# Performance work log

Measured on AMD Instinct MI355X. Metric: run time of the kernel, lower is better.

Reference implementation:

```python
import jax, jax.numpy as jnp
import numpy as np


def _gcn_conv(x, edge_index, W, b):
    # PyG GCNConv: linear transform, add self-loops, symmetric deg^{-1/2} norm,
    # scatter-add aggregation from source (row) into target (col), then bias.
    N = x.shape[0]
    h = x @ W  # [N, out]
    loops = jnp.arange(N, dtype=edge_index.dtype)
    row = jnp.concatenate([edge_index[0], loops])  # sources j
    col = jnp.concatenate([edge_index[1], loops])  # targets i
    deg = jax.ops.segment_sum(jnp.ones_like(col, dtype=h.dtype), col, num_segments=N)
    dinv = jnp.where(deg > 0, jax.lax.rsqrt(deg), 0.0)
    norm = dinv[row] * dinv[col]  # [E+N]
    msgs = norm[:, None] * h[row]  # gather + scale
    out = jax.ops.segment_sum(msgs, col, num_segments=N)  # scatter-add
    return out + b


def setup_inputs() -> dict:
    key = jax.random.key(0)
    k1, k2, k3, k4 = jax.random.split(key, 4)
    N, E, F, H = 100000, 3200000, 128, 64
    x = jax.random.normal(k1, (N, F), dtype=jnp.float32)
    edge_index = jax.random.randint(k2, (2, E), 0, N, dtype=jnp.int64)
    W1 = jax.random.normal(k3, (F, H), dtype=jnp.float32) * (1.0 / np.sqrt(F))
    b1 = jnp.zeros((H,), dtype=jnp.float32)
    W2 = jax.random.normal(k4, (H, 1), dtype=jnp.float32) * (1.0 / np.sqrt(H))
    b2 = jnp.zeros((1,), dtype=jnp.float32)
    return {"x": x, "edge_index": edge_index, "W1": W1, "b1": b1, "W2": W2, "b2": b2}


def reference(x, edge_index, W1, b1, W2, b2):
    # eval mode: dropout is identity
    h = _gcn_conv(x, edge_index, W1, b1)
    h = jax.nn.relu(h)
    h = _gcn_conv(h, edge_index, W2, b2)  # [N, 1]
    return jnp.mean(h, axis=0)  # [1]
```

## Files before the change

kernel.cpp:

```cpp
#include <hip/hip_runtime.h>
#include <hip/hip_bf16.h>
#include <stdint.h>


#define F_IN 128
#define H_DIM 64
#define BKT_SH 8
#define BKT_SZ 256
#define MAXBKT 512
#define PWG 256
#define PTHR 256
#define PPTHR 512
#define TILE 4096
#define CSR_CAP 10240
#define FINBLK 2048

typedef int   i4 __attribute__((ext_vector_type(4)));
typedef float f4 __attribute__((ext_vector_type(4)));
typedef float fv2 __attribute__((ext_vector_type(2)));

#if defined(__has_builtin)
#if __has_builtin(__builtin_amdgcn_cvt_pk_f32_fp8) && __has_builtin(__builtin_amdgcn_cvt_pk_fp8_f32)
#define HW_FP8 1
#endif
#endif

__device__ __forceinline__ float sw_dec_e4m3(unsigned b) {
    unsigned s = b & 0x80, e = (b >> 3) & 15, mm = b & 7;
    float v;
    if (e) v = __uint_as_float(((e + 120u) << 23) | (mm << 20));
    else   v = (float)mm * 0.001953125f;
    return s ? -v : v;
}
__device__ __forceinline__ unsigned sw_enc_e4m3(float f) {
    unsigned s = (__float_as_uint(f) & 0x80000000u) ? 0x80u : 0u;
    float a = fminf(fabsf(f), 448.0f);
    if (a < 9.765625e-4f) return s;
    if (a < 0.015625f) {
        int k = (int)rintf(a * 512.0f);
        if (k > 7) return s | 0x08;
        return s | (unsigned)k;
    }
    int e; float mant = frexpf(a, &e);
    int q = (int)rintf((mant * 2.0f - 1.0f) * 8.0f);
    int E = e - 1;
    if (q == 8) { q = 0; E += 1; }
    if (E > 8) { E = 8; q = 6; }
    return s | ((unsigned)(E + 7) << 3) | (unsigned)q;
}

__device__ __forceinline__ float2 f8pair(unsigned u) {
#ifdef HW_FP8
    fv2 r = __builtin_amdgcn_cvt_pk_f32_fp8((int)u, false);
    return make_float2(r.x, r.y);
#else
    return make_float2(sw_dec_e4m3(u & 0xff), sw_dec_e4m3((u >> 8) & 0xff));
#endif
}
__device__ __forceinline__ unsigned f8pack4(float v0, float v1, float v2, float v3) {
#ifdef HW_FP8
    unsigned pk = (unsigned)__builtin_amdgcn_cvt_pk_fp8_f32(v0, v1, 0, false);
    pk = (unsigned)__builtin_amdgcn_cvt_pk_fp8_f32(v2, v3, (int)pk, true);
    return pk;
#else
    return sw_enc_e4m3(v0) | (sw_enc_e4m3(v1) << 8) |
           (sw_enc_e4m3(v2) << 16) | (sw_enc_e4m3(v3) << 24);
#endif
}

__global__ __launch_bounds__(PTHR) void k_hist1(const int* __restrict__ col,
                                                int* __restrict__ histG,
                                                int E, int nbkt, int chunk) {
    __shared__ int h[MAXBKT];
    for (int i = threadIdx.x; i < nbkt; i += PTHR) h[i] = 0;
    __syncthreads();
    int s = blockIdx.x * chunk, e = min(E, s + chunk);
    if (s < e) {
        int s4 = s >> 2, e4 = e >> 2;
        const i4* c4 = (const i4*)col;
        int t = s4 + threadIdx.x;
        for (; t + 3 * PTHR < e4; t += 4 * PTHR) {
            i4 a = __builtin_nontemporal_load(c4 + t);
            i4 b = __builtin_nontemporal_load(c4 + t + PTHR);
            i4 c = __builtin_nontemporal_load(c4 + t + 2 * PTHR);
            i4 d = __builtin_nontemporal_load(c4 + t + 3 * PTHR);
            atomicAdd(&h[(unsigned)a.x >> BKT_SH], 1); atomicAdd(&h[(unsigned)a.y >> BKT_SH], 1);
            atomicAdd(&h[(unsigned)a.z >> BKT_SH], 1); atomicAdd(&h[(unsigned)a.w >> BKT_SH], 1);
            atomicAdd(&h[(unsigned)b.x >> BKT_SH], 1); atomicAdd(&h[(unsigned)b.y >> BKT_SH], 1);
            atomicAdd(&h[(unsigned)b.z >> BKT_SH], 1); atomicAdd(&h[(unsigned)b.w >> BKT_SH], 1);
            atomicAdd(&h[(unsigned)c.x >> BKT_SH], 1); atomicAdd(&h[(unsigned)c.y >> BKT_SH], 1);
            atomicAdd(&h[(unsigned)c.z >> BKT_SH], 1); atomicAdd(&h[(unsigned)c.w >> BKT_SH], 1);
            atomicAdd(&h[(unsigned)d.x >> BKT_SH], 1); atomicAdd(&h[(unsigned)d.y >> BKT_SH], 1);
            atomicAdd(&h[(unsigned)d.z >> BKT_SH], 1); atomicAdd(&h[(unsigned)d.w >> BKT_SH], 1);
        }
        for (; t < e4; t += PTHR) {
            i4 a = __builtin_nontemporal_load(c4 + t);
            atomicAdd(&h[(unsigned)a.x >> BKT_SH], 1); atomicAdd(&h[(unsigned)a.y >> BKT_SH], 1);
            atomicAdd(&h[(unsigned)a.z >> BKT_SH], 1); atomicAdd(&h[(unsigned)a.w >> BKT_SH], 1);
        }
        for (int i = (e4 << 2) + threadIdx.x; i < e; i += PTHR)
            atomicAdd(&h[(unsigned)col[i] >> BKT_SH], 1);
    }
    __syncthreads();
    for (int i = threadIdx.x; i < nbkt; i += PTHR)
        histG[(size_t)i * PWG + blockIdx.x] = h[i];
}

__global__ __launch_bounds__(PWG) void k_hscan_a(int* __restrict__ histG,
                                                 int* __restrict__ total, int nbkt) {
    __shared__ int s[PWG];
    int b = blockIdx.x, t = threadIdx.x;
    int v = histG[(size_t)b * PWG + t];
    s[t] = v;
    __syncthreads();
    for (int d = 1; d < PWG; d <<= 1) {
        int a = (t >= d) ? s[t - d] : 0;
        __syncthreads();
        s[t] += a;
        __syncthreads();
    }
    histG[(size_t)b * PWG + t] = s[t] - v;
    if (t == PWG - 1) total[b] = s[t];
}

__global__ __launch_bounds__(1024) void k_hscan_b(const int* __restrict__ total,
                                                  int* __restrict__ bstart, int nbkt) {
    __shared__ int s[1024];
    int t = threadIdx.x;
    int v = (t < nbkt) ? total[t] : 0;
    s[t] = v;
    __syncthreads();
    for (int d = 1; d < 1024; d <<= 1) {
        int a = (t >= d) ? s[t - d] : 0;
        __syncthreads();
        s[t] += a;
        __syncthreads();
    }
    if (t < nbkt) bstart[t] = s[t] - v;
    if (t == nbkt - 1) bstart[nbkt] = s[t];
}

__global__ __launch_bounds__(PPTHR) void k_part(const int* __restrict__ row,
                                                const int* __restrict__ col,
                                                const int* __restrict__ histG,
                                                const int* __restrict__ bstart,
                                                unsigned int* __restrict__ part,
                                                int E, int nbkt, int chunk) {
    __shared__ int hist[MAXBKT], hbase[MAXBKT], curl[MAXBKT], gcur[MAXBKT];
    __shared__ int ssc[PPTHR];
    __shared__ unsigned grouped[TILE];
    __shared__ ushort bkt16[TILE];
    int tid = threadIdx.x, wg = blockIdx.x;
    for (int i = tid; i < nbkt; i += PPTHR)
        gcur[i] = bstart[i] + histG[(size_t)i * PWG + wg];
    int s = wg * chunk, e = min(E, s + chunk);
    for (int ts = s; ts < e; ts += TILE) {
        int te = min(e, ts + TILE), tc = te - ts;
        for (int i = tid; i < nbkt; i += PPTHR) hist[i] = 0;
        __syncthreads();
        for (int i = ts + tid; i < te; i += PPTHR)
            atomicAdd(&hist[(unsigned)col[i] >> BKT_SH], 1);
        __syncthreads();
        int v = (tid < nbkt) ? hist[tid] : 0;
        ssc[tid] = v;
        __syncthreads();
        for (int d = 1; d < PPTHR; d <<= 1) {
            int a = (tid >= d) ? ssc[tid - d] : 0;
            __syncthreads();
            ssc[tid] += a;
            __syncthreads();
        }
        if (tid < nbkt) { hbase[tid] = ssc[tid] - v; curl[tid] = ssc[tid] - v; }
        __syncthreads();
        for (int i = ts + tid; i < te; i += PPTHR) {
            int c = col[i], r = row[i];
            int b = (unsigned)c >> BKT_SH;
            int p = atomicAdd(&curl[b], 1);
            grouped[p] = ((unsigned)r << BKT_SH) | (unsigned)(c & (BKT_SZ - 1));
            bkt16[p] = (ushort)b;
        }
        __syncthreads();
        for (int q = tid; q < tc; q += PPTHR) {
            int b = bkt16[q];
            part[gcur[b] + (q - hbase[b])] = grouped[q];
        }
        __syncthreads();
        for (int i = tid; i < nbkt; i += PPTHR) gcur[i] += hist[i];
        __syncthreads();
    }
}

__global__ __launch_bounds__(PTHR) void k_csr(const unsigned int* __restrict__ part,
                                              const int* __restrict__ bstart,
                                              int* __restrict__ offs,
                                              float* __restrict__ dinv,
                                              int* __restrict__ csr,
                                              int N, int E, int nbkt) {
    __shared__ int dg[BKT_SZ], sc[BKT_SZ], cur[BKT_SZ];
    __shared__ int stage[CSR_CAP];
    int b = blockIdx.x, tid = threadIdx.x;
    dg[tid] = 0;
    __syncthreads();
    int s = bstart[b], e = bstart[b + 1], cnt = e - s;
    for (int i = s + tid; i < e; i += PTHR)
        atomicAdd(&dg[part[i] & (BKT_SZ - 1)], 1);
    __syncthreads();
    int v = dg[tid];
    sc[tid] = v;
    __syncthreads();
    for (int d = 1; d < BKT_SZ; d <<= 1) {
        int a = (tid >= d) ? sc[tid - d] : 0;
        __syncthreads();
        sc[tid] += a;
        __syncthreads();
    }
    int ex = sc[tid] - v;
    cur[tid] = ex;
    int g = b * BKT_SZ + tid;
    if (g < N) {
        offs[g] = s + ex;
        dinv[g] = rsqrtf((float)v + 1.0f);
    }
    if (b == 0 && tid == 0) offs[N] = E;
    __syncthreads();
    if (cnt <= CSR_CAP) {
        for (int i = s + tid; i < e; i += PTHR) {
            unsigned u = part[i];
            int p = atomicAdd(&cur[u & (BKT_SZ - 1)], 1);
            stage[p] = (int)(u >> BKT_SH);
        }
        __syncthreads();
        for (int q = tid; q < cnt; q += PTHR)
            csr[s + q] = stage[q];
    } else {
        for (int i = s + tid; i < e; i += PTHR) {
            unsigned u = part[i];
            int p = atomicAdd(&cur[u & (BKT_SZ - 1)], 1);
            csr[s + p] = (int)(u >> BKT_SH);
        }
    }
}

__global__ __launch_bounds__(256) void k_gemm1(const float* __restrict__ x,
                                               const float* __restrict__ W1,
                                               const float* __restrict__ dinv,
                                               unsigned int* __restrict__ xw8,
                                               int N) {
    __shared__ float xs[64 * 132];
    __shared__ float ws[128 * 64];
    int tid = threadIdx.x;
    int row0 = blockIdx.x * 64;

    const float4* w4 = (const float4*)W1;
    float4* ws4 = (float4*)ws;
#pragma unroll
    for (int i = 0; i < 8; i++) ws4[tid + 256 * i] = w4[tid + 256 * i];

#pragma unroll
    for (int i = 0; i < 8; i++) {
        int idx = tid + 256 * i;
        int r = idx >> 5;
        int c = idx & 31;
        f4 v = {0.f, 0.f, 0.f, 0.f};
        int gr = row0 + r;
        if (gr < N) v = __builtin_nontemporal_load((const f4*)x + (size_t)gr * 32 + c);
        *(f4*)&xs[r * 132 + c * 4] = v;
    }
    __syncthreads();

    int tx = tid & 15, ty = tid >> 4;
    float acc[4][4] = {};
#pragma unroll 4
    for (int k = 0; k < 128; k++) {
        float4 wv = *(const float4*)&ws[k * 64 + tx * 4];
#pragma unroll
        for (int i = 0; i < 4; i++) {
            float xv = xs[(ty * 4 + i) * 132 + k];
            acc[i][0] += xv * wv.x;
            acc[i][1] += xv * wv.y;
            acc[i][2] += xv * wv.z;
            acc[i][3] += xv * wv.w;
        }
    }
#pragma unroll
    for (int i = 0; i < 4; i++) {
        int gr = row0 + ty * 4 + i;
        if (gr < N) {
            float dsc = dinv[gr];
            unsigned pk = f8pack4(acc[i][0] * dsc, acc[i][1] * dsc,
                                  acc[i][2] * dsc, acc[i][3] * dsc);
            xw8[(size_t)gr * 16 + tx] = pk;
        }
    }
}

__global__ __launch_bounds__(256) void k_agg(const ushort* __restrict__ xw8,
                                             const int* __restrict__ csr,
                                             const int* __restrict__ offs,
                                             const float* __restrict__ dinv,
                                             const float* __restrict__ b1,
                                             const float* __restrict__ W2,
                                             float* __restrict__ yp, int N) {
    int wid = (blockIdx.x * blockDim.x + threadIdx.x) >> 6;
    int lane = threadIdx.x & 63;
    if (wid >= N) return;
    int m = lane & 31, half = lane >> 5;

    float di = dinv[wid];
    float2 bv = ((const float2*)b1)[m];
    float2 wv = ((const float2*)W2)[m];

    float a0 = 0.f, a1 = 0.f;
    if (half == 0) {
        float2 sv = f8pair(xw8[(size_t)wid * 32 + m]);
        a0 += sv.x; a1 += sv.y;
    }
    int p = offs[wid], pe = offs[wid + 1];
    for (; p + 16 <= pe; p += 16) {
        int j0 = csr[p + 0 + half];
        int j1 = csr[p + 2 + half];
        int j2 = csr[p + 4 + half];
        int j3 = csr[p + 6 + half];
        int j4 = csr[p + 8 + half];
        int j5 = csr[p + 10 + half];
        int j6 = csr[p + 12 + half];
        int j7 = csr[p + 14 + half];
        ushort u0 = xw8[(size_t)j0 * 32 + m];
        ushort u1 = xw8[(size_t)j1 * 32 + m];
        ushort u2 = xw8[(size_t)j2 * 32 + m];
        ushort u3 = xw8[(size_t)j3 * 32 + m];
        ushort u4 = xw8[(size_t)j4 * 32 + m];
        ushort u5 = xw8[(size_t)j5 * 32 + m];
        ushort u6 = xw8[(size_t)j6 * 32 + m];
        ushort u7 = xw8[(size_t)j7 * 32 + m];
        float2 v0 = f8pair(u0), v1 = f8pair(u1), v2 = f8pair(u2), v3 = f8pair(u3);
        float2 v4 = f8pair(u4), v5 = f8pair(u5), v6 = f8pair(u6), v7 = f8pair(u7);
        a0 += ((v0.x + v1.x) + (v2.x + v3.x)) + ((v4.x + v5.x) + (v6.x + v7.x));
        a1 += ((v0.y + v1.y) + (v2.y + v3.y)) + ((v4.y + v5.y) + (v6.y + v7.y));
    }
    for (; p + 8 <= pe; p += 8) {
        int j0 = csr[p + 0 + half];
        int j1 = csr[p + 2 + half];
        int j2 = csr[p + 4 + half];
        int j3 = csr[p + 6 + half];
        float2 v0 = f8pair(xw8[(size_t)j0 * 32 + m]);
        float2 v1 = f8pair(xw8[(size_t)j1 * 32 + m]);
        float2 v2 = f8pair(xw8[(size_t)j2 * 32 + m]);
        float2 v3 = f8pair(xw8[(size_t)j3 * 32 + m]);
        a0 += (v0.x + v1.x) + (v2.x + v3.x);
        a1 += (v0.y + v1.y) + (v2.y + v3.y);
    }
    for (; p + 2 <= pe; p += 2) {
        int j = csr[p + half];
        float2 v = f8pair(xw8[(size_t)j * 32 + m]);
        a0 += v.x; a1 += v.y;
    }
    if (p < pe && half == 0) {
        int j = csr[p];
        float2 v = f8pair(xw8[(size_t)j * 32 + m]);
        a0 += v.x; a1 += v.y;
    }
    a0 += __shfl_xor(a0, 32, 64);
    a1 += __shfl_xor(a1, 32, 64);
    float h0 = fmaxf(bv.x + di * a0, 0.f);
    float h1 = fmaxf(bv.y + di * a1, 0.f);
    float v = h0 * wv.x + h1 * wv.y;
#pragma unroll
    for (int d = 16; d > 0; d >>= 1) v += __shfl_xor(v, d, 64);
    if (lane == 0) yp[wid] = di * v;
}

__global__ __launch_bounds__(256) void k_final2(const int* __restrict__ csr,
                                                const int* __restrict__ offs,
                                                const float* __restrict__ dinv,
                                                const float* __restrict__ yp,
                                                float* __restrict__ partial, int N) {
    int lane = threadIdx.x & 63, w = threadIdx.x >> 6;
    int nwave_tot = gridDim.x * 4;
    int wid0 = blockIdx.x * 4 + w;
    float wpart = 0.f;
    for (int i = wid0; i < N; i += nwave_tot) {
        int p0 = offs[i], p1 = offs[i + 1];
        float s = (lane == 0) ? yp[i] : 0.f;
        for (int p = p0 + lane; p < p1; p += 64)
            s += yp[csr[p]];
#pragma unroll
        for (int d = 32; d > 0; d >>= 1) s += __shfl_xor(s, d, 64);
        if (lane == 0) wpart += dinv[i] * s;
    }
    __shared__ float wsum[4];
    if (lane == 0) wsum[w] = wpart;
    __syncthreads();
    if (threadIdx.x == 0)
        partial[blockIdx.x] = (wsum[0] + wsum[1]) + (wsum[2] + wsum[3]);
}

__global__ __launch_bounds__(256) void k_write(const float* __restrict__ partial,
                                               const float* __restrict__ b2,
                                               float* __restrict__ out, int nb, int N) {
    float s = 0.f;
    for (int i = threadIdx.x; i < nb; i += 256) s += partial[i];
#pragma unroll
    for (int d = 32; d > 0; d >>= 1) s += __shfl_xor(s, d, 64);
    __shared__ float wsum[4];
    int lane = threadIdx.x & 63, w = threadIdx.x >> 6;
    if (lane == 0) wsum[w] = s;
    __syncthreads();
    if (threadIdx.x == 0)
        out[0] = b2[0] + ((wsum[0] + wsum[1]) + (wsum[2] + wsum[3])) / (float)N;
}

extern "C" void kernel_launch(void* const* d_in, const int* in_sizes, int n_in,
                              void* d_out, int out_size, void* d_ws, size_t ws_size,
                              hipStream_t stream) {
    const float* x  = (const float*)d_in[0];
    const int*   ei = (const int*)d_in[1];
    const float* W1 = (const float*)d_in[2];
    const float* b1 = (const float*)d_in[3];
    const float* W2 = (const float*)d_in[4];
    const float* b2 = (const float*)d_in[5];

    int N = in_sizes[0] / F_IN;
    int E = in_sizes[1] / 2;
    const int* erow = ei;
    const int* ecol = ei + E;

    int NBKT = (N + BKT_SZ - 1) >> BKT_SH;
    int chunk = (((E + PWG - 1) / PWG) + 3) & ~3;

    char* w = (char*)d_ws;
    auto take = [&](size_t bytes) {
        char* p = w;
        w += (bytes + 255) & ~(size_t)255;
        return p;
    };
    int*          histG   = (int*)take((size_t)NBKT * PWG * 4);
    int*          total   = (int*)take((size_t)NBKT * 4);
    int*          bstart  = (int*)take((size_t)(NBKT + 1) * 4);
    unsigned int* part    = (unsigned int*)take((size_t)E * 4);
    int*          csr     = (int*)take((size_t)E * 4);
    int*          offs    = (int*)take((size_t)(N + 1) * 4);
    float*        dinv    = (float*)take((size_t)N * 4);
    float*        yp      = (float*)take((size_t)N * 4);
    float*        partial = (float*)take((size_t)FINBLK * 4);
    unsigned int* xw8     = (unsigned int*)take((size_t)N * H_DIM);
    (void)ws_size;

    float* out = (float*)d_out;

    k_hist1<<<PWG, PTHR, 0, stream>>>(ecol, histG, E, NBKT, chunk);
    k_hscan_a<<<NBKT, PWG, 0, stream>>>(histG, total, NBKT);
    k_hscan_b<<<1, 1024, 0, stream>>>(total, bstart, NBKT);
    k_part<<<PWG, PPTHR, 0, stream>>>(erow, ecol, histG, bstart, part, E, NBKT, chunk);
    k_csr<<<NBKT, PTHR, 0, stream>>>(part, bstart, offs, dinv, csr, N, E, NBKT);
    k_gemm1<<<(N + 63) / 64, 256, 0, stream>>>(x, W1, dinv, xw8, N);
    k_agg<<<((size_t)N * 64 + 255) / 256, 256, 0, stream>>>((const ushort*)xw8, csr, offs, dinv, b1, W2, yp, N);
    k_final2<<<FINBLK, 256, 0, stream>>>(csr, offs, dinv, yp, partial, N);
    k_write<<<1, 256, 0, stream>>>(partial, b2, out, FINBLK, N);
}
```

Before: 195.6 us.

## Replace per-node final gather with multi-pass LDS-tiled edge-stream reduction

The final layer-2 reduction no longer walks the CSR per node. k_csr now writes a per-edge value, the target node's dinv. A small kernel converts yp to bf16 and adds the self-loop terms. Several passes of k_fedge then stream all edges (part plus zval), each pass holding a slice of about 25.6K bf16 yp values in LDS and summing only the edges whose source falls in that slice. This swaps random global/L2 gathers for LDS lookups. The cost is re-reading the full edge list once per pass, an extra E-sized float array and bf16 rounding of yp.

```diff
diff --git a/kernel.cpp b/kernel.cpp
--- a/kernel.cpp
+++ b/kernel.cpp
@@ -13,7 +13,9 @@
 #define PPTHR 512
 #define TILE 4096
 #define CSR_CAP 10240
-#define FINBLK 2048
+#define QCAP 25600
+#define FEDGE_WGS 256
+#define PARTMAX 2048
 
 typedef int   i4 __attribute__((ext_vector_type(4)));
 typedef float f4 __attribute__((ext_vector_type(4)));
@@ -66,6 +68,14 @@
     return sw_enc_e4m3(v0) | (sw_enc_e4m3(v1) << 8) |
            (sw_enc_e4m3(v2) << 16) | (sw_enc_e4m3(v3) << 24);
 #endif
+}
+
+__device__ __forceinline__ ushort f2bf(float v) {
+    unsigned u = __float_as_uint(v);
+    return (ushort)((u + 0x7fffu + ((u >> 16) & 1u)) >> 16);
+}
+__device__ __forceinline__ float bf2f(ushort b) {
+    return __uint_as_float(((unsigned)b) << 16);
 }
 
 __global__ __launch_bounds__(PTHR) void k_hist1(const int* __restrict__ col,
@@ -195,8 +205,10 @@
                                               int* __restrict__ offs,
                                               float* __restrict__ dinv,
                                               int* __restrict__ csr,
+                                              float* __restrict__ zval,
                                               int N, int E, int nbkt) {
     __shared__ int dg[BKT_SZ], sc[BKT_SZ], cur[BKT_SZ];
+    __shared__ float sdinv[BKT_SZ];
     __shared__ int stage[CSR_CAP];
     int b = blockIdx.x, tid = threadIdx.x;
     dg[tid] = 0;
@@ -216,17 +228,21 @@
     }
     int ex = sc[tid] - v;
     cur[tid] = ex;
+    float dv = rsqrtf((float)v + 1.0f);
+    sdinv[tid] = dv;
     int g = b * BKT_SZ + tid;
     if (g < N) {
         offs[g] = s + ex;
-        dinv[g] = rsqrtf((float)v + 1.0f);
+        dinv[g] = dv;
     }
     if (b == 0 && tid == 0) offs[N] = E;
     __syncthreads();
     if (cnt <= CSR_CAP) {
         for (int i = s + tid; i < e; i += PTHR) {
             unsigned u = part[i];
-            int p = atomicAdd(&cur[u & (BKT_SZ - 1)], 1);
+            int cl = u & (BKT_SZ - 1);
+            zval[i] = sdinv[cl];
+            int p = atomicAdd(&cur[cl], 1);
             stage[p] = (int)(u >> BKT_SH);
         }
         __syncthreads();
@@ -235,7 +251,9 @@
     } else {
         for (int i = s + tid; i < e; i += PTHR) {
             unsigned u = part[i];
-            int p = atomicAdd(&cur[u & (BKT_SZ - 1)], 1);
+            int cl = u & (BKT_SZ - 1);
+            zval[i] = sdinv[cl];
+            int p = atomicAdd(&cur[cl], 1);
             csr[s + p] = (int)(u >> BKT_SH);
         }
     }
@@ -370,29 +388,69 @@
     if (lane == 0) yp[wid] = di * v;
 }
 
-__global__ __launch_bounds__(256) void k_final2(const int* __restrict__ csr,
-                                                const int* __restrict__ offs,
-                                                const float* __restrict__ dinv,
-                                                const float* __restrict__ yp,
-                                                float* __restrict__ partial, int N) {
+__global__ __launch_bounds__(256) void k_cvt(const float* __restrict__ yp,
+                                             const float* __restrict__ dinv,
+                                             ushort* __restrict__ yph,
+                                             float* __restrict__ partial, int N) {
+    int i = blockIdx.x * 256 + threadIdx.x;
+    float local = 0.f;
+    if (i < N) {
+        float v = yp[i];
+        yph[i] = f2bf(v);
+        local = dinv[i] * v;
+    }
+#pragma unroll
+    for (int d = 32; d > 0; d >>= 1) local += __shfl_xor(local, d, 64);
+    __shared__ float wsum[4];
     int lane = threadIdx.x & 63, w = threadIdx.x >> 6;
-    int nwave_tot = gridDim.x * 4;
-    int wid0 = blockIdx.x * 4 + w;
-    float wpart = 0.f;
-    for (int i = wid0; i < N; i += nwave_tot) {
-        int p0 = offs[i], p1 = offs[i + 1];
-        float s = (lane == 0) ? yp[i] : 0.f;
-        for (int p = p0 + lane; p < p1; p += 64)
-            s += yp[csr[p]];
-#pragma unroll
-        for (int d = 32; d > 0; d >>= 1) s += __shfl_xor(s, d, 64);
-        if (lane == 0) wpart += dinv[i] * s;
-    }
-    __shared__ float wsum[4];
-    if (lane == 0) wsum[w] = wpart;
+    if (lane == 0) wsum[w] = local;
     __syncthreads();
     if (threadIdx.x == 0)
         partial[blockIdx.x] = (wsum[0] + wsum[1]) + (wsum[2] + wsum[3]);
+}
+
+__global__ __launch_bounds__(512) void k_fedge(const unsigned int* __restrict__ part,
+                                               const float* __restrict__ zval,
+                                               const ushort* __restrict__ yph,
+                                               float* __restrict__ partial,
+                                               int E, int N, int base, int pOff) {
+    __shared__ ushort ylds[QCAP];
+    int hi = min(N - base, QCAP);
+    for (int i = threadIdx.x; i < hi; i += 512) ylds[i] = yph[base + i];
+    __syncthreads();
+    float local = 0.f;
+    int tid = blockIdx.x * 512 + threadIdx.x;
+    int nthr = gridDim.x * 512;
+    int E4 = E >> 2;
+    const i4* p4 = (const i4*)part;
+    const f4* z4 = (const f4*)zval;
+    for (int t = tid; t < E4; t += nthr) {
+        i4 u = __builtin_nontemporal_load(p4 + t);
+        f4 z = __builtin_nontemporal_load(z4 + t);
+        int r0 = (int)((unsigned)u.x >> BKT_SH) - base;
+        int r1 = (int)((unsigned)u.y >> BKT_SH) - base;
+        int r2 = (int)((unsigned)u.z >> BKT_SH) - base;
+        int r3 = (int)((unsigned)u.w >> BKT_SH) - base;
+        if ((unsigned)r0 < (unsigned)hi) local += bf2f(ylds[r0]) * z.x;
+        if ((unsigned)r1 < (unsigned)hi) local += bf2f(ylds[r1]) * z.y;
+        if ((unsigned)r2 < (unsigned)hi) local += bf2f(ylds[r2]) * z.z;
+        if ((unsigned)r3 < (unsigned)hi) local += bf2f(ylds[r3]) * z.w;
+    }
+    for (int e = (E4 << 2) + tid; e < E; e += nthr) {
+        int r = (int)(part[e] >> BKT_SH) - base;
+        if ((unsigned)r < (unsigned)hi) local += bf2f(ylds[r]) * zval[e];
+    }
+#pragma unroll
+    for (int d = 32; d > 0; d >>= 1) local += __shfl_xor(local, d, 64);
+    __shared__ float wsum[8];
+    int lane = threadIdx.x & 63, w = threadIdx.x >> 6;
+    if (lane == 0) wsum[w] = local;
+    __syncthreads();
+    if (threadIdx.x == 0) {
+        float s = ((wsum[0] + wsum[1]) + (wsum[2] + wsum[3]))
+                + ((wsum[4] + wsum[5]) + (wsum[6] + wsum[7]));
+        partial[pOff + blockIdx.x] = s;
+    }
 }
 
 __global__ __launch_bounds__(256) void k_write(const float* __restrict__ partial,
@@ -439,22 +497,30 @@
     int*          bstart  = (int*)take((size_t)(NBKT + 1) * 4);
     unsigned int* part    = (unsigned int*)take((size_t)E * 4);
     int*          csr     = (int*)take((size_t)E * 4);
+    float*        zval    = (float*)take((size_t)E * 4);
     int*          offs    = (int*)take((size_t)(N + 1) * 4);
     float*        dinv    = (float*)take((size_t)N * 4);
     float*        yp      = (float*)take((size_t)N * 4);
-    float*        partial = (float*)take((size_t)FINBLK * 4);
+    ushort*       yph     = (ushort*)take((size_t)N * 2);
+    float*        partial = (float*)take((size_t)PARTMAX * 4);
     unsigned int* xw8     = (unsigned int*)take((size_t)N * H_DIM);
     (void)ws_size;
 
     float* out = (float*)d_out;
+
+    int cvtB = (N + 255) / 256;
+    int npass = (N + QCAP - 1) / QCAP;
 
     k_hist1<<<PWG, PTHR, 0, stream>>>(ecol, histG, E, NBKT, chunk);
     k_hscan_a<<<NBKT, PWG, 0, stream>>>(histG, total, NBKT);
     k_hscan_b<<<1, 1024, 0, stream>>>(total, bstart, NBKT);
     k_part<<<PWG, PPTHR, 0, stream>>>(erow, ecol, histG, bstart, part, E, NBKT, chunk);
-    k_csr<<<NBKT, PTHR, 0, stream>>>(part, bstart, offs, dinv, csr, N, E, NBKT);
+    k_csr<<<NBKT, PTHR, 0, stream>>>(part, bstart, offs, dinv, csr, zval, N, E, NBKT);
     k_gemm1<<<(N + 63) / 64, 256, 0, stream>>>(x, W1, dinv, xw8, N);
     k_agg<<<((size_t)N * 64 + 255) / 256, 256, 0, stream>>>((const ushort*)xw8, csr, offs, dinv, b1, W2, yp, N);
-    k_final2<<<FINBLK, 256, 0, stream>>>(csr, offs, dinv, yp, partial, N);
-    k_write<<<1, 256, 0, stream>>>(partial, b2, out, FINBLK, N);
-}
+    k_cvt<<<cvtB, 256, 0, stream>>>(yp, dinv, yph, partial, N);
+    for (int p = 0; p < npass; p++)
+        k_fedge<<<FEDGE_WGS, 512, 0, stream>>>(part, zval, yph, partial,
+                                               E, N, p * QCAP, cvtB + p * FEDGE_WGS);
+    k_write<<<1, 256, 0, stream>>>(partial, b2, out, cvtB + npass * FEDGE_WGS, N);
+}
```

Result: slower. 218.3 us (+11.6%).

## Replace layer-2 gather with source-bucketed scatter using precomputed per-edge target dinv

Applied to the files above, without the earlier changes.

The final layer's mean only needs sum over nodes of yp[j] times the summed target dinv over j's out-edges, plus the self-loop term. The change builds a second partition of edges keyed by source bucket, packing each edge's target dinv as bf16. A per-bucket shared-memory reduction then replaces the per-target random gather of yp. This adds a second histogram, scan and partition pass over E edges plus extra workspace, and rounds per-edge weights to bf16.

```diff
diff --git a/kernel.cpp b/kernel.cpp
--- a/kernel.cpp
+++ b/kernel.cpp
@@ -13,7 +13,7 @@
 #define PPTHR 512
 #define TILE 4096
 #define CSR_CAP 10240
-#define FINBLK 2048
+#define PARTMAX 2048
 
 typedef int   i4 __attribute__((ext_vector_type(4)));
 typedef float f4 __attribute__((ext_vector_type(4)));
@@ -66,6 +66,14 @@
     return sw_enc_e4m3(v0) | (sw_enc_e4m3(v1) << 8) |
            (sw_enc_e4m3(v2) << 16) | (sw_enc_e4m3(v3) << 24);
 #endif
+}
+
+__device__ __forceinline__ ushort f2bf(float v) {
+    unsigned u = __float_as_uint(v);
+    return (ushort)((u + 0x7fffu + ((u >> 16) & 1u)) >> 16);
+}
+__device__ __forceinline__ float bf2f(ushort b) {
+    return __uint_as_float(((unsigned)b) << 16);
 }
 
 __global__ __launch_bounds__(PTHR) void k_hist1(const int* __restrict__ col,
@@ -106,6 +114,30 @@
         histG[(size_t)i * PWG + blockIdx.x] = h[i];
 }
 
+__global__ __launch_bounds__(PTHR) void k_hist2(const unsigned int* __restrict__ part,
+                                                int* __restrict__ histG,
+                                                int E, int nbkt, int chunk) {
+    __shared__ int h[MAXBKT];
+    for (int i = threadIdx.x; i < nbkt; i += PTHR) h[i] = 0;
+    __syncthreads();
+    int s = blockIdx.x * chunk, e = min(E, s + chunk);
+    if (s < e) {
+        int s4 = s >> 2, e4 = e >> 2;
+        const i4* c4 = (const i4*)part;
+        int t = s4 + threadIdx.x;
+        for (; t < e4; t += PTHR) {
+            i4 a = __builtin_nontemporal_load(c4 + t);
+            atomicAdd(&h[(unsigned)a.x >> 16], 1); atomicAdd(&h[(unsigned)a.y >> 16], 1);
+            atomicAdd(&h[(unsigned)a.z >> 16], 1); atomicAdd(&h[(unsigned)a.w >> 16], 1);
+        }
+        for (int i = (e4 << 2) + threadIdx.x; i < e; i += PTHR)
+            atomicAdd(&h[part[i] >> 16], 1);
+    }
+    __syncthreads();
+    for (int i = threadIdx.x; i < nbkt; i += PTHR)
+        histG[(size_t)i * PWG + blockIdx.x] = h[i];
+}
+
 __global__ __launch_bounds__(PWG) void k_hscan_a(int* __restrict__ histG,
                                                  int* __restrict__ total, int nbkt) {
     __shared__ int s[PWG];
@@ -190,13 +222,66 @@
     }
 }
 
+__global__ __launch_bounds__(PPTHR) void k_part2(const unsigned int* __restrict__ part,
+                                                 const float* __restrict__ zval,
+                                                 const int* __restrict__ histG,
+                                                 const int* __restrict__ bstart,
+                                                 unsigned int* __restrict__ epk,
+                                                 int E, int nbkt, int chunk) {
+    __shared__ int hist[MAXBKT], hbase[MAXBKT], curl[MAXBKT], gcur[MAXBKT];
+    __shared__ int ssc[PPTHR];
+    __shared__ unsigned grouped[TILE];
+    __shared__ ushort bkt16[TILE];
+    int tid = threadIdx.x, wg = blockIdx.x;
+    for (int i = tid; i < nbkt; i += PPTHR)
+        gcur[i] = bstart[i] + histG[(size_t)i * PWG + wg];
+    int s = wg * chunk, e = min(E, s + chunk);
+    for (int ts = s; ts < e; ts += TILE) {
+        int te = min(e, ts + TILE), tc = te - ts;
+        for (int i = tid; i < nbkt; i += PPTHR) hist[i] = 0;
+        __syncthreads();
+        for (int i = ts + tid; i < te; i += PPTHR)
+            atomicAdd(&hist[part[i] >> 16], 1);
+        __syncthreads();
+        int v = (tid < nbkt) ? hist[tid] : 0;
+        ssc[tid] = v;
+        __syncthreads();
+        for (int d = 1; d < PPTHR; d <<= 1) {
+            int a = (tid >= d) ? ssc[tid - d] : 0;
+            __syncthreads();
+            ssc[tid] += a;
+            __syncthreads();
+        }
+        if (tid < nbkt) { hbase[tid] = ssc[tid] - v; curl[tid] = ssc[tid] - v; }
+        __syncthreads();
+        for (int i = ts + tid; i < te; i += PPTHR) {
+            unsigned u = part[i];
+            int b = u >> 16;
+            unsigned rl = (u >> BKT_SH) & (BKT_SZ - 1);
+            int p = atomicAdd(&curl[b], 1);
+            grouped[p] = (rl << 16) | (unsigned)f2bf(zval[i]);
+            bkt16[p] = (ushort)b;
+        }
+        __syncthreads();
+        for (int q = tid; q < tc; q += PPTHR) {
+            int b = bkt16[q];
+            epk[gcur[b] + (q - hbase[b])] = grouped[q];
+        }
+        __syncthreads();
+        for (int i = tid; i < nbkt; i += PPTHR) gcur[i] += hist[i];
+        __syncthreads();
+    }
+}
+
 __global__ __launch_bounds__(PTHR) void k_csr(const unsigned int* __restrict__ part,
                                               const int* __restrict__ bstart,
                                               int* __restrict__ offs,
                                               float* __restrict__ dinv,
                                               int* __restrict__ csr,
+                                              float* __restrict__ zval,
                                               int N, int E, int nbkt) {
     __shared__ int dg[BKT_SZ], sc[BKT_SZ], cur[BKT_SZ];
+    __shared__ float sdinv[BKT_SZ];
     __shared__ int stage[CSR_CAP];
     int b = blockIdx.x, tid = threadIdx.x;
     dg[tid] = 0;
@@ -216,17 +301,21 @@
     }
     int ex = sc[tid] - v;
     cur[tid] = ex;
+    float dv = rsqrtf((float)v + 1.0f);
+    sdinv[tid] = dv;
     int g = b * BKT_SZ + tid;
     if (g < N) {
         offs[g] = s + ex;
-        dinv[g] = rsqrtf((float)v + 1.0f);
+        dinv[g] = dv;
     }
     if (b == 0 && tid == 0) offs[N] = E;
     __syncthreads();
     if (cnt <= CSR_CAP) {
         for (int i = s + tid; i < e; i += PTHR) {
             unsigned u = part[i];
-            int p = atomicAdd(&cur[u & (BKT_SZ - 1)], 1);
+            int cl = u & (BKT_SZ - 1);
+            zval[i] = sdinv[cl];
+            int p = atomicAdd(&cur[cl], 1);
             stage[p] = (int)(u >> BKT_SH);
         }
         __syncthreads();
@@ -235,7 +324,9 @@
     } else {
         for (int i = s + tid; i < e; i += PTHR) {
             unsigned u = part[i];
-            int p = atomicAdd(&cur[u & (BKT_SZ - 1)], 1);
+            int cl = u & (BKT_SZ - 1);
+            zval[i] = sdinv[cl];
+            int p = atomicAdd(&cur[cl], 1);
             csr[s + p] = (int)(u >> BKT_SH);
         }
     }
@@ -370,29 +461,31 @@
     if (lane == 0) yp[wid] = di * v;
 }
 
-__global__ __launch_bounds__(256) void k_final2(const int* __restrict__ csr,
-                                                const int* __restrict__ offs,
-                                                const float* __restrict__ dinv,
-                                                const float* __restrict__ yp,
-                                                float* __restrict__ partial, int N) {
-    int lane = threadIdx.x & 63, w = threadIdx.x >> 6;
-    int nwave_tot = gridDim.x * 4;
-    int wid0 = blockIdx.x * 4 + w;
-    float wpart = 0.f;
-    for (int i = wid0; i < N; i += nwave_tot) {
-        int p0 = offs[i], p1 = offs[i + 1];
-        float s = (lane == 0) ? yp[i] : 0.f;
-        for (int p = p0 + lane; p < p1; p += 64)
-            s += yp[csr[p]];
-#pragma unroll
-        for (int d = 32; d > 0; d >>= 1) s += __shfl_xor(s, d, 64);
-        if (lane == 0) wpart += dinv[i] * s;
-    }
+__global__ __launch_bounds__(PTHR) void k_srcsum(const unsigned int* __restrict__ epk,
+                                                 const int* __restrict__ bstart2,
+                                                 const float* __restrict__ dinv,
+                                                 const float* __restrict__ yp,
+                                                 float* __restrict__ partial, int N) {
+    __shared__ float acc[BKT_SZ];
+    int b = blockIdx.x, tid = threadIdx.x;
+    acc[tid] = 0.f;
+    __syncthreads();
+    int s = bstart2[b], e = bstart2[b + 1];
+    for (int i = s + tid; i < e; i += PTHR) {
+        unsigned u = epk[i];
+        atomicAdd(&acc[u >> 16], bf2f((ushort)(u & 0xffffu)));
+    }
+    __syncthreads();
+    int g = b * BKT_SZ + tid;
+    float local = 0.f;
+    if (g < N) local = (acc[tid] + dinv[g]) * yp[g];
+#pragma unroll
+    for (int d = 32; d > 0; d >>= 1) local += __shfl_xor(local, d, 64);
     __shared__ float wsum[4];
-    if (lane == 0) wsum[w] = wpart;
-    __syncthreads();
-    if (threadIdx.x == 0)
-        partial[blockIdx.x] = (wsum[0] + wsum[1]) + (wsum[2] + wsum[3]);
+    int lane = tid & 63, w = tid >> 6;
+    if (lane == 0) wsum[w] = local;
+    __syncthreads();
+    if (tid == 0) partial[b] = (wsum[0] + wsum[1]) + (wsum[2] + wsum[3]);
 }
 
 __global__ __launch_bounds__(256) void k_write(const float* __restrict__ partial,
@@ -435,14 +528,19 @@
         return p;
     };
     int*          histG   = (int*)take((size_t)NBKT * PWG * 4);
+    int*          histG2  = (int*)take((size_t)NBKT * PWG * 4);
     int*          total   = (int*)take((size_t)NBKT * 4);
+    int*          total2  = (int*)take((size_t)NBKT * 4);
     int*          bstart  = (int*)take((size_t)(NBKT + 1) * 4);
+    int*          bstart2 = (int*)take((size_t)(NBKT + 1) * 4);
     unsigned int* part    = (unsigned int*)take((size_t)E * 4);
+    unsigned int* epk     = (unsigned int*)take((size_t)E * 4);
     int*          csr     = (int*)take((size_t)E * 4);
+    float*        zval    = (float*)take((size_t)E * 4);
     int*          offs    = (int*)take((size_t)(N + 1) * 4);
     float*        dinv    = (float*)take((size_t)N * 4);
     float*        yp      = (float*)take((size_t)N * 4);
-    float*        partial = (float*)take((size_t)FINBLK * 4);
+    float*        partial = (float*)take((size_t)PARTMAX * 4);
     unsigned int* xw8     = (unsigned int*)take((size_t)N * H_DIM);
     (void)ws_size;
 
@@ -452,9 +550,13 @@
     k_hscan_a<<<NBKT, PWG, 0, stream>>>(histG, total, NBKT);
     k_hscan_b<<<1, 1024, 0, stream>>>(total, bstart, NBKT);
     k_part<<<PWG, PPTHR, 0, stream>>>(erow, ecol, histG, bstart, part, E, NBKT, chunk);
-    k_csr<<<NBKT, PTHR, 0, stream>>>(part, bstart, offs, dinv, csr, N, E, NBKT);
+    k_csr<<<NBKT, PTHR, 0, stream>>>(part, bstart, offs, dinv, csr, zval, N, E, NBKT);
+    k_hist2<<<PWG, PTHR, 0, stream>>>(part, histG2, E, NBKT, chunk);
+    k_hscan_a<<<NBKT, PWG, 0, stream>>>(histG2, total2, NBKT);
+    k_hscan_b<<<1, 1024, 0, stream>>>(total2, bstart2, NBKT);
+    k_part2<<<PWG, PPTHR, 0, stream>>>(part, zval, histG2, bstart2, epk, E, NBKT, chunk);
     k_gemm1<<<(N + 63) / 64, 256, 0, stream>>>(x, W1, dinv, xw8, N);
     k_agg<<<((size_t)N * 64 + 255) / 256, 256, 0, stream>>>((const ushort*)xw8, csr, offs, dinv, b1, W2, yp, N);
-    k_final2<<<FINBLK, 256, 0, stream>>>(csr, offs, dinv, yp, partial, N);
-    k_write<<<1, 256, 0, stream>>>(partial, b2, out, FINBLK, N);
-}
+    k_srcsum<<<NBKT, PTHR, 0, stream>>>(epk, bstart2, dinv, yp, partial, N);
+    k_write<<<1, 256, 0, stream>>>(partial, b2, out, NBKT, N);
+}
```

After: 243.9 us. 24.7% more time.
